# Performance work log

Hardware: AMD Instinct MI355X
Metric: run time of the kernel (lower is better)

Reference implementation:

```python
import jax, jax.numpy as jnp
import numpy as np

N_NODES = 100000
N_EDGES = 1600000
D_IN = 128
D_OUT = 128


def setup_inputs() -> dict:
    key = jax.random.key(0)
    k_x, k_e, k_wl, k_bl, k_wr = jax.random.split(key, 5)
    x = jax.random.normal(k_x, (N_NODES, D_IN), dtype=jnp.float32)
    edge_index = jax.random.randint(k_e, (2, N_EDGES), 0, N_NODES, dtype=jnp.int64)
    s = 1.0 / np.sqrt(D_IN)
    W_l = jax.random.uniform(k_wl, (D_OUT, D_IN), minval=-s, maxval=s, dtype=jnp.float32)
    b_l = jax.random.uniform(k_bl, (D_OUT,), minval=-s, maxval=s, dtype=jnp.float32)
    W_r = jax.random.uniform(k_wr, (D_OUT, D_IN), minval=-s, maxval=s, dtype=jnp.float32)
    return {"x": x, "edge_index": edge_index, "W_l": W_l, "b_l": b_l, "W_r": W_r}


def reference(x, edge_index, W_l, b_l, W_r):
    # PyG SAGEConv with mean aggregation:
    #   out = lin_l(mean_{j in N(i)} x_j) + lin_r(x_i), followed by ReLU.
    src, dst = edge_index[0], edge_index[1]
    # gather source features [E, D_IN] and mean-aggregate at destinations
    msg_sum = jax.ops.segment_sum(x[src], dst, num_segments=N_NODES)  # [N, D_IN]
    deg = jax.ops.segment_sum(jnp.ones((edge_index.shape[1],), dtype=x.dtype), dst,
                              num_segments=N_NODES)  # [N]
    agg = msg_sum / jnp.maximum(deg, 1.0)[:, None]  # isolated nodes -> 0
    out = agg @ W_l.T + b_l + x @ W_r.T
    return jax.nn.relu(out)
```

## Files before the change

### kernel.cpp

```cpp
#include <hip/hip_runtime.h>
#include <hip/hip_bf16.h>
#include <cstddef>
#include <cstdint>

#define D 128
#define BCHUNK 4096
#define SLOTS 64
#define TILE 128
#define LROW 68
#define SBCAP 5120
#define NGMAX 512

typedef __bf16 bf16x8 __attribute__((ext_vector_type(8)));
typedef float  f32x4  __attribute__((ext_vector_type(4)));
typedef float  f32x2  __attribute__((ext_vector_type(2)));

__device__ __forceinline__ unsigned int f2bf(float f) {
    unsigned int u = __float_as_uint(f);
    return (u + 0x7FFFu + ((u >> 16) & 1u)) >> 16;
}

__global__ __launch_bounds__(256) void bucketx2_kernel(
    const int* __restrict__ ei, int E, int* __restrict__ subCnt,
    unsigned int* __restrict__ sub, int NG, int nbE, int nbX,
    const float4* __restrict__ x4, uint2* __restrict__ xb2,
    unsigned int* __restrict__ xg, int nq,
    const float* __restrict__ Wl, const float* __restrict__ Wr,
    const float* __restrict__ bl, unsigned short* __restrict__ bfrag,
    float* __restrict__ biasbuf)
{
    const int bid = blockIdx.x;
    if (bid >= nbE) {
        const int xi = bid - nbE;
        if (xi < nbX) {
            const int base = xi * 1024 + threadIdx.x;
            #pragma unroll
            for (int k = 0; k < 4; k++) {
                int i = base + k * 256;
                if (i < nq) {
                    float4 v = x4[i];
                    uint2 r;
                    r.x = f2bf(v.x) | (f2bf(v.y) << 16);
                    r.y = f2bf(v.z) | (f2bf(v.w) << 16);
                    xb2[i] = r;
                    int g = 0;
                    g = __builtin_amdgcn_cvt_pk_fp8_f32(v.x, v.y, g, false);
                    g = __builtin_amdgcn_cvt_pk_fp8_f32(v.z, v.w, g, true);
                    xg[(size_t)((i >> 5) + 1) * 32 + (i & 31)] = (unsigned int)g;
                }
            }
        } else {
            int f = (xi - nbX) * 256 + threadIdx.x;
            if (f < 4096) {
                int ct   = f >> 9;
                int q    = (f >> 6) & 7;
                int lane = f & 63;
                int o  = 16 * ct + (lane & 15);
                int kb = 32 * q + (lane >> 4) * 8;
                const float* s = (kb < 128) ? (Wl + (size_t)o * 128 + kb)
                                            : (Wr + (size_t)o * 128 + (kb - 128));
                uint4 u;
                u.x = f2bf(s[0]) | (f2bf(s[1]) << 16);
                u.y = f2bf(s[2]) | (f2bf(s[3]) << 16);
                u.z = f2bf(s[4]) | (f2bf(s[5]) << 16);
                u.w = f2bf(s[6]) | (f2bf(s[7]) << 16);
                reinterpret_cast<uint4*>(bfrag)[f] = u;
                if (f < 128) biasbuf[f] = bl[f];
                if (f < 32)  xg[f] = 0u;
            }
        }
        return;
    }
    __shared__ int cnt[NGMAX], base[NGMAX], posl[NGMAX];
    for (int i = threadIdx.x; i < NG; i += 256) { cnt[i] = 0; posl[i] = 0; }
    __syncthreads();
    const int cb = bid * BCHUNK;
    int srcs[16], gs[16], d8s[16];
    #pragma unroll
    for (int k = 0; k < 16; k++) {
        int e = cb + threadIdx.x + k * 256;
        bool v = e < E;
        srcs[k] = v ? ei[e] : 0;
        int dst = v ? ei[E + e] : 0;
        gs[k]  = v ? (dst >> 8) : -1;
        d8s[k] = dst & 255;
        if (v) atomicAdd(&cnt[gs[k]], 1);
    }
    __syncthreads();
    for (int i = threadIdx.x; i < NG; i += 256)
        base[i] = (cnt[i] > 0) ? atomicAdd(&subCnt[i], cnt[i]) : 0;
    __syncthreads();
    #pragma unroll
    for (int k = 0; k < 16; k++) {
        if (gs[k] >= 0) {
            int pos = base[gs[k]] + atomicAdd(&posl[gs[k]], 1);
            if (pos < SBCAP)
                sub[(size_t)gs[k] * SBCAP + pos] =
                    (unsigned int)(srcs[k] + 1) | ((unsigned int)d8s[k] << 20);
        }
    }
}

__global__ __launch_bounds__(256) void csrg_kernel(
    const unsigned int* __restrict__ sub, const int* __restrict__ subCnt,
    int* __restrict__ csr, int* __restrict__ deg, int N)
{
    __shared__ int lcnt[256];
    const int g = blockIdx.x;
    const int n = min(subCnt[g], SBCAP);
    lcnt[threadIdx.x] = 0;
    __syncthreads();
    const unsigned int* S = sub + (size_t)g * SBCAP;
    const int nbase = g << 8;
    for (int i = threadIdx.x; i < n; i += 256) {
        unsigned int en = S[i];
        int d8  = (en >> 20) & 255;
        int pos = atomicAdd(&lcnt[d8], 1);
        if (pos < SLOTS)
            csr[(size_t)(nbase + d8) * SLOTS + pos] = (int)(en & 0xFFFFFu);
    }
    __syncthreads();
    int node = nbase + threadIdx.x;
    if (node < N) deg[node] = lcnt[threadIdx.x];
}

__global__ __launch_bounds__(512) void gathformer_kernel(
    const int* __restrict__ deg_, const int* __restrict__ csr,
    const unsigned int* __restrict__ xg, const unsigned int* __restrict__ xb,
    const unsigned short* __restrict__ bfrag, const float* __restrict__ biasbuf,
    float* __restrict__ out, int N)
{
    __shared__ unsigned int lds[TILE * LROW];

    const int w    = threadIdx.x >> 6;
    const int lane = threadIdx.x & 63;
    const int sub  = lane & 31;
    const int half = lane >> 5;
    const int node0 = blockIdx.x * TILE;

    for (int i = 0; i < 16; i++) {
        int node = node0 + w * 16 + i;
        if (node >= N) break;
        int deg = deg_[node];
        int dl  = min(deg, SLOTS);
        int nbatch = (dl + 15) >> 4;
        const int* nb = csr + (size_t)node * SLOTS;
        f32x2 a01 = {0.f, 0.f};
        f32x2 a23 = {0.f, 0.f};
        for (int b = 0; b < nbatch; b++) {
            const int j = b * 16;
            unsigned int v[8];
            #pragma unroll
            for (int u = 0; u < 8; u++) {
                int slot = j + 2 * u + half;
                int raw  = nb[slot];
                int s    = (slot < dl) ? raw : 0;
                v[u] = xg[(size_t)s * 32 + sub];
            }
            #pragma unroll
            for (int u = 0; u < 8; u++) {
                a01 += __builtin_amdgcn_cvt_pk_f32_fp8(v[u], false);
                a23 += __builtin_amdgcn_cvt_pk_f32_fp8(v[u], true);
            }
        }
        a01.x += __shfl_xor(a01.x, 32);
        a01.y += __shfl_xor(a01.y, 32);
        a23.x += __shfl_xor(a23.x, 32);
        a23.y += __shfl_xor(a23.y, 32);
        if (half == 0) {
            float inv = 1.0f / fmaxf((float)deg, 1.0f);
            int b = (w * 16 + i) * LROW + sub * 2;
            lds[b]     = f2bf(a01.x * inv) | (f2bf(a01.y * inv) << 16);
            lds[b + 1] = f2bf(a23.x * inv) | (f2bf(a23.y * inv) << 16);
        }
    }
    __syncthreads();

    const int quad = lane >> 4;
    const int r15  = lane & 15;
    bf16x8 bw[8];
    #pragma unroll
    for (int q = 0; q < 8; q++)
        bw[q] = reinterpret_cast<const bf16x8*>(bfrag)[(w * 8 + q) * 64 + lane];
    const float bias = biasbuf[16 * w + r15];
    const int col = 16 * w + r15;

    #pragma unroll 1
    for (int mt = 0; mt < 8; mt++) {
        int rowbase = node0 + mt * 16;
        if (rowbase >= N) break;
        int rc = min(rowbase + r15, N - 1);
        f32x4 acc = {0.f, 0.f, 0.f, 0.f};
        const int lbase = (mt * 16 + r15) * LROW + quad * 4;
        #pragma unroll
        for (int q = 0; q < 4; q++) {
            bf16x8 a = *reinterpret_cast<const bf16x8*>(&lds[lbase + q * 16]);
            acc = __builtin_amdgcn_mfma_f32_16x16x32_bf16(a, bw[q], acc, 0, 0, 0);
        }
        const unsigned short* xrow =
            (const unsigned short*)xb + (size_t)rc * 128 + quad * 8;
        #pragma unroll
        for (int q = 4; q < 8; q++) {
            bf16x8 a = *reinterpret_cast<const bf16x8*>(xrow + (q - 4) * 32);
            acc = __builtin_amdgcn_mfma_f32_16x16x32_bf16(a, bw[q], acc, 0, 0, 0);
        }
        #pragma unroll
        for (int r = 0; r < 4; r++) {
            int orow = rowbase + quad * 4 + r;
            if (orow < N)
                out[(size_t)orow * D + col] = fmaxf(acc[r] + bias, 0.0f);
        }
    }
}

extern "C" void kernel_launch(void* const* d_in, const int* in_sizes, int n_in,
                              void* d_out, int out_size, void* d_ws, size_t ws_size,
                              hipStream_t stream)
{
    const float* x  = (const float*)d_in[0];
    const int*   ei = (const int*)d_in[1];
    const float* Wl = (const float*)d_in[2];
    const float* bl = (const float*)d_in[3];
    const float* Wr = (const float*)d_in[4];
    float* out = (float*)d_out;

    const int nodes = in_sizes[0] / D;
    const int E     = in_sizes[1] / 2;
    const int NG    = (nodes + 255) >> 8;

    int* deg         = (int*)d_ws;
    unsigned int* xg = (unsigned int*)(deg + nodes);
    int* csr         = (int*)(xg + (size_t)(nodes + 1) * 32);
    unsigned int* xb = (unsigned int*)(csr + (size_t)nodes * SLOTS);
    unsigned short* bfrag = (unsigned short*)(xb + (size_t)nodes * 64);
    float* biasbuf   = (float*)(bfrag + 4096 * 8);
    int* subCnt      = (int*)(biasbuf + 128);
    unsigned int* sub = (unsigned int*)d_out;

    hipMemsetAsync(subCnt, 0, (size_t)NG * sizeof(int), stream);

    const int nbE = (E + BCHUNK - 1) / BCHUNK;
    const int nq  = nodes * 32;
    const int nbX = (nq + 1023) / 1024;
    bucketx2_kernel<<<nbE + nbX + 16, 256, 0, stream>>>(
        ei, E, subCnt, sub, NG, nbE, nbX,
        (const float4*)x, (uint2*)xb, xg, nq, Wl, Wr, bl, bfrag, biasbuf);

    csrg_kernel<<<NG, 256, 0, stream>>>(sub, subCnt, csr, deg, nodes);

    gathformer_kernel<<<(nodes + TILE - 1) / TILE, 512, 0, stream>>>(
        deg, csr, xg, xb, bfrag, biasbuf, out, nodes);
}
```

Baseline: 222.3 us.

## Fuse CSR construction into gather kernel using shared-memory per-tile adjacency

Removes the separate csrg kernel and the global CSR/degree arrays. Each gather block now scans its 256-node group's bucket list, keeps only entries for its own 64-node quarter, and builds the neighbour lists and degrees in LDS. This drops a kernel launch and the global write and read-back of the CSR. In exchange every bucket list is read four times, the tile shrinks to 64 nodes, and the bucket buffer moves from the output buffer into the workspace.

```diff
diff --git a/kernel.cpp b/kernel.cpp
--- a/kernel.cpp
+++ b/kernel.cpp
@@ -6,7 +6,7 @@
 #define D 128
 #define BCHUNK 4096
 #define SLOTS 64
-#define TILE 128
+#define QTILE 64
 #define LROW 68
 #define SBCAP 5120
 #define NGMAX 512
@@ -101,50 +101,48 @@
     }
 }
 
-__global__ __launch_bounds__(256) void csrg_kernel(
+__global__ __launch_bounds__(512) void gathformer_kernel(
     const unsigned int* __restrict__ sub, const int* __restrict__ subCnt,
-    int* __restrict__ csr, int* __restrict__ deg, int N)
-{
-    __shared__ int lcnt[256];
-    const int g = blockIdx.x;
-    const int n = min(subCnt[g], SBCAP);
-    lcnt[threadIdx.x] = 0;
-    __syncthreads();
-    const unsigned int* S = sub + (size_t)g * SBCAP;
-    const int nbase = g << 8;
-    for (int i = threadIdx.x; i < n; i += 256) {
-        unsigned int en = S[i];
-        int d8  = (en >> 20) & 255;
-        int pos = atomicAdd(&lcnt[d8], 1);
-        if (pos < SLOTS)
-            csr[(size_t)(nbase + d8) * SLOTS + pos] = (int)(en & 0xFFFFFu);
-    }
-    __syncthreads();
-    int node = nbase + threadIdx.x;
-    if (node < N) deg[node] = lcnt[threadIdx.x];
-}
-
-__global__ __launch_bounds__(512) void gathformer_kernel(
-    const int* __restrict__ deg_, const int* __restrict__ csr,
     const unsigned int* __restrict__ xg, const unsigned int* __restrict__ xb,
     const unsigned short* __restrict__ bfrag, const float* __restrict__ biasbuf,
     float* __restrict__ out, int N)
 {
-    __shared__ unsigned int lds[TILE * LROW];
+    __shared__ unsigned int lds[QTILE * LROW];
+    __shared__ int lcsr[QTILE * SLOTS];
+    __shared__ int lcnt[QTILE];
+
+    const int g     = blockIdx.x >> 2;
+    const int h     = blockIdx.x & 3;
+    const int node0 = (g << 8) + (h << 6);
 
     const int w    = threadIdx.x >> 6;
     const int lane = threadIdx.x & 63;
-    const int sub  = lane & 31;
+    const int sb   = lane & 31;
     const int half = lane >> 5;
-    const int node0 = blockIdx.x * TILE;
-
-    for (int i = 0; i < 16; i++) {
-        int node = node0 + w * 16 + i;
+
+    if (threadIdx.x < QTILE) lcnt[threadIdx.x] = 0;
+    __syncthreads();
+    const int n = min(subCnt[g], SBCAP);
+    const unsigned int* S = sub + (size_t)g * SBCAP;
+    for (int i = threadIdx.x; i < n; i += 512) {
+        unsigned int en = S[i];
+        int d8 = (en >> 20) & 255;
+        if ((d8 >> 6) == h) {
+            int ln  = d8 & 63;
+            int pos = atomicAdd(&lcnt[ln], 1);
+            if (pos < SLOTS) lcsr[ln * SLOTS + pos] = (int)(en & 0xFFFFFu);
+        }
+    }
+    __syncthreads();
+
+    for (int i = 0; i < 8; i++) {
+        int ln   = w * 8 + i;
+        int node = node0 + ln;
         if (node >= N) break;
-        int deg = deg_[node];
+        int deg = lcnt[ln];
         int dl  = min(deg, SLOTS);
         int nbatch = (dl + 15) >> 4;
-        const int* nb = csr + (size_t)node * SLOTS;
+        const int* nb = lcsr + ln * SLOTS;
         f32x2 a01 = {0.f, 0.f};
         f32x2 a23 = {0.f, 0.f};
         for (int b = 0; b < nbatch; b++) {
@@ -155,7 +153,7 @@
                 int slot = j + 2 * u + half;
                 int raw  = nb[slot];
                 int s    = (slot < dl) ? raw : 0;
-                v[u] = xg[(size_t)s * 32 + sub];
+                v[u] = xg[(size_t)s * 32 + sb];
             }
             #pragma unroll
             for (int u = 0; u < 8; u++) {
@@ -169,7 +167,7 @@
         a23.y += __shfl_xor(a23.y, 32);
         if (half == 0) {
             float inv = 1.0f / fmaxf((float)deg, 1.0f);
-            int b = (w * 16 + i) * LROW + sub * 2;
+            int b = ln * LROW + sb * 2;
             lds[b]     = f2bf(a01.x * inv) | (f2bf(a01.y * inv) << 16);
             lds[b + 1] = f2bf(a23.x * inv) | (f2bf(a23.y * inv) << 16);
         }
@@ -186,7 +184,7 @@
     const int col = 16 * w + r15;
 
     #pragma unroll 1
-    for (int mt = 0; mt < 8; mt++) {
+    for (int mt = 0; mt < 4; mt++) {
         int rowbase = node0 + mt * 16;
         if (rowbase >= N) break;
         int rc = min(rowbase + r15, N - 1);
@@ -228,14 +226,12 @@
     const int E     = in_sizes[1] / 2;
     const int NG    = (nodes + 255) >> 8;
 
-    int* deg         = (int*)d_ws;
-    unsigned int* xg = (unsigned int*)(deg + nodes);
-    int* csr         = (int*)(xg + (size_t)(nodes + 1) * 32);
-    unsigned int* xb = (unsigned int*)(csr + (size_t)nodes * SLOTS);
+    unsigned int* xg = (unsigned int*)d_ws;
+    unsigned int* xb = xg + (size_t)(nodes + 1) * 32;
     unsigned short* bfrag = (unsigned short*)(xb + (size_t)nodes * 64);
     float* biasbuf   = (float*)(bfrag + 4096 * 8);
     int* subCnt      = (int*)(biasbuf + 128);
-    unsigned int* sub = (unsigned int*)d_out;
+    unsigned int* sub = (unsigned int*)(subCnt + 512);
 
     hipMemsetAsync(subCnt, 0, (size_t)NG * sizeof(int), stream);
 
@@ -246,8 +242,6 @@
         ei, E, subCnt, sub, NG, nbE, nbX,
         (const float4*)x, (uint2*)xb, xg, nq, Wl, Wr, bl, bfrag, biasbuf);
 
-    csrg_kernel<<<NG, 256, 0, stream>>>(sub, subCnt, csr, deg, nodes);
-
-    gathformer_kernel<<<(nodes + TILE - 1) / TILE, 512, 0, stream>>>(
-        deg, csr, xg, xb, bfrag, biasbuf, out, nodes);
-}
+    gathformer_kernel<<<NG * 4, 512, 0, stream>>>(
+        sub, subCnt, xg, xb, bfrag, biasbuf, out, nodes);
+}
```

After: 191.4 us. -13.9%, faster.
